# Kernel tuning notes

Hardware: AMD Instinct MI355X
Metric: run time of the kernel (lower is better)

## Reference

```python
import jax, jax.numpy as jnp
import numpy as np
import math

D, NH, DFF = 1024, 16, 4096
B, S = 2, 2048
EPS = 1e-5


def _mha(q_in, k_in, v_in, wq, bq, wk, bk, wv, bv, wo, bo, mask):
    Bq, Sq, Dm = q_in.shape
    Sk = k_in.shape[1]
    dh = Dm // NH
    q = (q_in @ wq + bq).reshape(Bq, Sq, NH, dh).transpose(0, 2, 1, 3)
    k = (k_in @ wk + bk).reshape(Bq, Sk, NH, dh).transpose(0, 2, 1, 3)
    v = (v_in @ wv + bv).reshape(Bq, Sk, NH, dh).transpose(0, 2, 1, 3)
    scores = jnp.einsum('bhqd,bhkd->bhqk', q, k) / math.sqrt(dh)
    scores = jnp.where(mask == 0, jnp.float32(-1e9), scores)
    w = jax.nn.softmax(scores, axis=-1)
    out = jnp.einsum('bhqk,bhkd->bhqd', w, v)
    out = out.transpose(0, 2, 1, 3).reshape(Bq, Sq, Dm)
    return out @ wo + bo


def _ln(x, g, b):
    mu = jnp.mean(x, axis=-1, keepdims=True)
    var = jnp.var(x, axis=-1, keepdims=True)
    return (x - mu) * jax.lax.rsqrt(var + EPS) * g + b


def setup_inputs() -> dict:
    key = jax.random.key(0)
    ks = jax.random.split(key, 20)
    sc = 1.0 / math.sqrt(D)
    inp = {
        'x': jax.random.normal(ks[0], (B, S, D), jnp.float32),
        'encoder_output': jax.random.normal(ks[1], (B, S, D), jnp.float32),
        'src_mask': jnp.ones((B, 1, 1, S), jnp.int32),
        'tgt_mask': jnp.tril(jnp.ones((S, S), jnp.int32))[None, None],
    }
    names = ['s_wq', 's_wk', 's_wv', 's_wo', 'c_wq', 'c_wk', 'c_wv', 'c_wo']
    for i, n in enumerate(names):
        inp[n] = jax.random.normal(ks[2 + i], (D, D), jnp.float32) * sc
        inp[n.replace('w', 'b')] = jnp.zeros((D,), jnp.float32)
    inp['ff_w1'] = jax.random.normal(ks[10], (D, DFF), jnp.float32) * sc
    inp['ff_b1'] = jnp.zeros((DFF,), jnp.float32)
    inp['ff_w2'] = jax.random.normal(ks[11], (DFF, D), jnp.float32) / math.sqrt(DFF)
    inp['ff_b2'] = jnp.zeros((D,), jnp.float32)
    for i in (1, 2, 3):
        inp[f'ln{i}_g'] = jnp.ones((D,), jnp.float32)
        inp[f'ln{i}_b'] = jnp.zeros((D,), jnp.float32)
    return inp


def reference(x, encoder_output, src_mask, tgt_mask,
              s_wq, s_bq, s_wk, s_bk, s_wv, s_bv, s_wo, s_bo,
              c_wq, c_bq, c_wk, c_bk, c_wv, c_bv, c_wo, c_bo,
              ff_w1, ff_b1, ff_w2, ff_b2,
              ln1_g, ln1_b, ln2_g, ln2_b, ln3_g, ln3_b):
    # self-attention + residual + LN (dropout is identity in eval)
    a = _mha(x, x, x, s_wq, s_bq, s_wk, s_bk, s_wv, s_bv, s_wo, s_bo, tgt_mask)
    x = _ln(x + a, ln1_g, ln1_b)
    # cross-attention
    a = _mha(x, encoder_output, encoder_output,
             c_wq, c_bq, c_wk, c_bk, c_wv, c_bv, c_wo, c_bo, src_mask)
    x = _ln(x + a, ln2_g, ln2_b)
    # FFN
    f = jax.nn.relu(x @ ff_w1 + ff_b1) @ ff_w2 + ff_b2
    return _ln(x + f, ln3_g, ln3_b)
```

## Files before the change

kernel.cpp:

```cpp
#include <hip/hip_runtime.h>
#include <hip/hip_bf16.h>
#include <stdint.h>


#define DEV static __device__ __forceinline__

typedef short bf16s;
typedef __attribute__((ext_vector_type(8))) short bf16x8;
typedef __attribute__((ext_vector_type(4))) float f32x4;

DEV short f2b(float f) {
    union { __hip_bfloat16 h; short s; } u;
    u.h = __float2bfloat16(f);
    return u.s;
}

DEV f32x4 mfma16(bf16x8 a, bf16x8 b, f32x4 c) {
    return __builtin_amdgcn_mfma_f32_16x16x32_bf16(a, b, c, 0, 0, 0);
}

DEV void gload_lds16(const bf16s* g, short* l) {
    __builtin_amdgcn_global_load_lds(
        (const __attribute__((address_space(1))) void*)g,
        (__attribute__((address_space(3))) void*)l,
        16, 0, 0);
}

__global__ __launch_bounds__(256) void cast2_f32_bf16_kernel(
    const float* __restrict__ a, const float* __restrict__ b,
    bf16s* __restrict__ out, int n)
{
    int i = (blockIdx.x * 256 + threadIdx.x) * 8;
    const float* src = (i < n) ? a : b;
    int j = (i < n) ? i : i - n;
    const float4 u = *(const float4*)(src + j);
    const float4 v = *(const float4*)(src + j + 4);
    bf16x8 r;
    r[0] = f2b(u.x); r[1] = f2b(u.y); r[2] = f2b(u.z); r[3] = f2b(u.w);
    r[4] = f2b(v.x); r[5] = f2b(v.y); r[6] = f2b(v.z); r[7] = f2b(v.w);
    *(bf16x8*)(out + i) = r;
}

struct P8 { const float* p[8]; };

__global__ __launch_bounds__(256) void transpose_cast8_kernel(
    P8 srcs, bf16s* __restrict__ dst)
{
    __shared__ short tile[64][65];
    const float* W = srcs.p[blockIdx.z];
    bf16s* Wt = dst + (size_t)blockIdx.z * 1024 * 1024;
    const int n0 = blockIdx.x * 64, k0 = blockIdx.y * 64;
    const int t = threadIdx.x;
#pragma unroll
    for (int it = 0; it < 16; ++it) {
        int idx = it * 256 + t;
        int r = idx >> 6, c = idx & 63;
        tile[r][c] = f2b(W[(size_t)(k0 + r) * 1024 + n0 + c]);
    }
    __syncthreads();
#pragma unroll
    for (int it = 0; it < 16; ++it) {
        int idx = it * 256 + t;
        int r = idx >> 6, c = idx & 63;
        Wt[(size_t)(n0 + r) * 1024 + k0 + c] = tile[c][r];
    }
}

__global__ __launch_bounds__(256) void transpose_cast_kernel(
    const float* __restrict__ W, bf16s* __restrict__ Wt, int Krows, int Ncols)
{
    __shared__ short tile[64][65];
    const int n0 = blockIdx.x * 64, k0 = blockIdx.y * 64;
    const int t = threadIdx.x;
#pragma unroll
    for (int it = 0; it < 16; ++it) {
        int idx = it * 256 + t;
        int r = idx >> 6, c = idx & 63;
        tile[r][c] = f2b(W[(size_t)(k0 + r) * Ncols + n0 + c]);
    }
    __syncthreads();
#pragma unroll
    for (int it = 0; it < 16; ++it) {
        int idx = it * 256 + t;
        int r = idx >> 6, c = idx & 63;
        Wt[(size_t)(n0 + r) * Krows + k0 + c] = tile[c][r];
    }
}

__global__ __launch_bounds__(256) void transpose_v_kernel(
    const bf16s* __restrict__ V, int ldv, bf16s* __restrict__ Vt, int Sk)
{
    __shared__ short tile[64][65];
    const int s0 = blockIdx.x * 64;
    const int bh = blockIdx.y, b = bh >> 4, h = bh & 15;
    const int t = threadIdx.x;
#pragma unroll
    for (int it = 0; it < 16; ++it) {
        int idx = it * 256 + t;
        int r = idx >> 6, c = idx & 63;
        tile[r][c] = V[(size_t)(b * Sk + s0 + r) * ldv + h * 64 + c];
    }
    __syncthreads();
#pragma unroll
    for (int it = 0; it < 16; ++it) {
        int idx = it * 256 + t;
        int r = idx >> 6, c = idx & 63;
        Vt[((size_t)bh * 64 + r) * Sk + s0 + c] = tile[c][r];
    }
}

__global__ void concat3_kernel(const float* a, const float* b, const float* c,
                               float* o, int n)
{
    int i = blockIdx.x * 256 + threadIdx.x;
    if (i < n) { o[i] = a[i]; o[n + i] = b[i]; o[2 * n + i] = c[i]; }
}
__global__ void concat2_kernel(const float* a, const float* b, float* o, int n)
{
    int i = blockIdx.x * 256 + threadIdx.x;
    if (i < n) { o[i] = a[i]; o[n + i] = b[i]; }
}

template<int BM, int OUT_BF16, int RELU>
__global__ __launch_bounds__(256, (BM == 64 ? 4 : 2))
void gemm_bt_kernel(const bf16s* __restrict__ A, const bf16s* __restrict__ Bt,
                    const float* __restrict__ bias, void* __restrict__ Cp,
                    int M, int N, int K)
{
    constexpr int BN = 128;
    constexpr int WR = BM / 64;
    constexpr int WC = 4 / WR;
    constexpr int TN = BN / WC;
    constexpr int NF = TN / 16;
    constexpr int RA = BM / 64;
    constexpr int ASZ = BM * 32;

    __shared__ short As[2 * ASZ];
    __shared__ short Bs[2 * BN * 32];

    const int t = threadIdx.x, lane = t & 63, wave = t >> 6;
    const int g = lane >> 4, ln16 = lane & 15;
    const int wr = wave / WC, wc = wave % WC;
    const int rowA0 = blockIdx.y * BM, rowB0 = blockIdx.x * BN;

    const bf16s* Ab = A + (size_t)rowA0 * K;
    const bf16s* Bb = Bt + (size_t)rowB0 * K;

    f32x4 acc[4][NF] = {};

    auto stage = [&](int buf, int k0) {
        short* Ad = As + buf * ASZ;
        short* Bd = Bs + buf * BN * 32;
#pragma unroll
        for (int rnd = 0; rnd < RA; ++rnd) {
            int p = rnd * 256 + t;
            int sr = p >> 3, c3 = (p & 7) ^ (sr & 7);
            int r = sr * 2 + (c3 >> 2), c = c3 & 3;
            gload_lds16(Ab + (size_t)r * K + k0 + c * 8,
                        Ad + (rnd * 256 + wave * 64) * 8);
        }
#pragma unroll
        for (int rnd = 0; rnd < 2; ++rnd) {
            int p = rnd * 256 + t;
            int sr = p >> 3, c3 = (p & 7) ^ (sr & 7);
            int r = sr * 2 + (c3 >> 2), c = c3 & 3;
            gload_lds16(Bb + (size_t)r * K + k0 + c * 8,
                        Bd + (rnd * 256 + wave * 64) * 8);
        }
    };

    stage(0, 0);
    __syncthreads();
    int cur = 0;
    for (int k0 = 0; k0 < K; k0 += 32) {
        if (k0 + 32 < K) stage(cur ^ 1, k0 + 32);
        const short* Ar = As + cur * ASZ;
        const short* Br = Bs + cur * BN * 32;
        bf16x8 af[4], bfr[NF];
#pragma unroll
        for (int m = 0; m < 4; ++m) {
            int r = wr * 64 + m * 16 + ln16;
            int sr = r >> 1, c3 = (r & 1) * 4 + g;
            af[m] = *(const bf16x8*)(Ar + sr * 64 + ((c3 ^ (sr & 7)) * 8));
        }
#pragma unroll
        for (int n = 0; n < NF; ++n) {
            int r = wc * TN + n * 16 + ln16;
            int sr = r >> 1, c3 = (r & 1) * 4 + g;
            bfr[n] = *(const bf16x8*)(Br + sr * 64 + ((c3 ^ (sr & 7)) * 8));
        }
#pragma unroll
        for (int m = 0; m < 4; ++m)
#pragma unroll
            for (int n = 0; n < NF; ++n)
                acc[m][n] = mfma16(af[m], bfr[n], acc[m][n]);
        __syncthreads();
        cur ^= 1;
    }

    const int row0 = rowA0 + wr * 64, col0 = rowB0 + wc * TN;
#pragma unroll
    for (int n = 0; n < NF; ++n) {
        const int col = col0 + n * 16 + ln16;
        const float bv = bias[col];
#pragma unroll
        for (int m = 0; m < 4; ++m) {
#pragma unroll
            for (int r = 0; r < 4; ++r) {
                int row = row0 + m * 16 + g * 4 + r;
                float v = acc[m][n][r] + bv;
                if (RELU) v = fmaxf(v, 0.f);
                if (OUT_BF16) ((bf16s*)Cp)[(size_t)row * N + col] = f2b(v);
                else          ((float*)Cp)[(size_t)row * N + col] = v;
            }
        }
    }
}

template<int CAUSAL>
__global__ __launch_bounds__(256, 4)
void flash_kernel(const bf16s* __restrict__ Q, int ldq,
                  const bf16s* __restrict__ K, int ldk,
                  const bf16s* __restrict__ Vt,
                  bf16s* __restrict__ O, int ldo,
                  int Sq, int Sk, float scale)
{
    __shared__ short Ks[2 * 64 * 64];
    __shared__ short Vs[2 * 64 * 64];
    __shared__ short Ps[4 * 16 * 64];
    const int t = threadIdx.x, lane = t & 63, wave = t >> 6;
    const int g = lane >> 4, ln16 = lane & 15;
    const int qt = CAUSAL ? (int)(gridDim.x - 1 - blockIdx.x) : (int)blockIdx.x;
    const int bh = blockIdx.y, b = bh >> 4, h = bh & 15;
    const int q0 = qt * 64;
    const float sc2 = scale * 1.44269504f;

    bf16x8 aq[2];
    {
        const size_t qrow = (size_t)(b * Sq + q0 + wave * 16 + ln16);
#pragma unroll
        for (int kk = 0; kk < 2; ++kk)
            aq[kk] = *(const bf16x8*)(Q + qrow * ldq + h * 64 + kk * 32 + g * 8);
    }

    float m_r[4], l_r[4];
    f32x4 oa[4] = {};
#pragma unroll
    for (int r = 0; r < 4; ++r) { m_r[r] = -1e30f; l_r[r] = 0.f; }

    const int nkt = CAUSAL ? (qt + 1) : (Sk >> 6);
    const bf16s* Kbase = K + (size_t)b * Sk * ldk + h * 64;
    const bf16s* Vbase = Vt + (size_t)bh * 64 * Sk;
    short* myP = Ps + wave * 1024;

    auto stage = [&](int buf, int kt) {
        const bf16s* ksrc = Kbase + (size_t)(kt * 64) * ldk;
        const bf16s* vsrc = Vbase + kt * 64;
        short* Kd = Ks + buf * 4096;
        short* Vd = Vs + buf * 4096;
#pragma unroll
        for (int rnd = 0; rnd < 2; ++rnd) {
            int p = rnd * 256 + t;
            int r = p >> 3, c = (p & 7) ^ (r & 7);
            gload_lds16(ksrc + (size_t)r * ldk + c * 8,
                        Kd + (rnd * 256 + wave * 64) * 8);
        }
#pragma unroll
        for (int rnd = 0; rnd < 2; ++rnd) {
            int p = rnd * 256 + t;
            int r = p >> 3, c = (p & 7) ^ (r & 7);
            gload_lds16(vsrc + (size_t)r * Sk + c * 8,
                        Vd + (rnd * 256 + wave * 64) * 8);
        }
    };

    stage(0, 0);
    __syncthreads();
    int cur = 0;

    for (int kt = 0; kt < nkt; ++kt) {
        if (kt + 1 < nkt) stage(cur ^ 1, kt + 1);
        const short* Kr = Ks + cur * 4096;
        const short* Vr = Vs + cur * 4096;

        f32x4 sa[4] = {};
#pragma unroll
        for (int kk = 0; kk < 2; ++kk) {
#pragma unroll
            for (int n = 0; n < 4; ++n) {
                int key = n * 16 + ln16;
                bf16x8 bk = *(const bf16x8*)(Kr + key * 64 +
                                             (((kk * 4 + g) ^ (key & 7)) * 8));
                sa[n] = mfma16(aq[kk], bk, sa[n]);
            }
        }

        const bool diag = CAUSAL && (kt == qt);
        float sv[4][4];
#pragma unroll
        for (int n = 0; n < 4; ++n) {
#pragma unroll
            for (int r = 0; r < 4; ++r) {
                float s = sa[n][r] * sc2;
                if (diag) {
                    int kl = n * 16 + ln16, ql = wave * 16 + g * 4 + r;
                    if (kl > ql) s = -1e30f;
                }
                sv[n][r] = s;
            }
        }

        float rm[4];
#pragma unroll
        for (int r = 0; r < 4; ++r)
            rm[r] = fmaxf(fmaxf(sv[0][r], sv[1][r]), fmaxf(sv[2][r], sv[3][r]));
#pragma unroll
        for (int x = 1; x < 16; x <<= 1)
#pragma unroll
            for (int r = 0; r < 4; ++r)
                rm[r] = fmaxf(rm[r], __shfl_xor(rm[r], x, 64));

        float al[4];
#pragma unroll
        for (int r = 0; r < 4; ++r) {
            float mn = fmaxf(m_r[r], rm[r]);
            al[r] = exp2f(m_r[r] - mn);
            m_r[r] = mn;
        }
        float rs[4] = {0.f, 0.f, 0.f, 0.f};
#pragma unroll
        for (int n = 0; n < 4; ++n)
#pragma unroll
            for (int r = 0; r < 4; ++r) {
                float p = exp2f(sv[n][r] - m_r[r]);
                sv[n][r] = p;
                rs[r] += p;
            }
#pragma unroll
        for (int x = 1; x < 16; x <<= 1)
#pragma unroll
            for (int r = 0; r < 4; ++r)
                rs[r] += __shfl_xor(rs[r], x, 64);
#pragma unroll
        for (int r = 0; r < 4; ++r)
            l_r[r] = l_r[r] * al[r] + rs[r];

#pragma unroll
        for (int n = 0; n < 4; ++n)
#pragma unroll
            for (int r = 0; r < 4; ++r) {
                int row = g * 4 + r, col = n * 16 + ln16;
                myP[row * 64 + (((col >> 3) ^ (row & 7)) * 8) + (col & 7)] =
                    f2b(sv[n][r]);
            }
        asm volatile("s_waitcnt lgkmcnt(0)" ::: "memory");

#pragma unroll
        for (int n = 0; n < 4; ++n)
#pragma unroll
            for (int r = 0; r < 4; ++r)
                oa[n][r] *= al[r];
#pragma unroll
        for (int kk = 0; kk < 2; ++kk) {
            bf16x8 pa = *(const bf16x8*)(myP + ln16 * 64 +
                                         (((kk * 4 + g) ^ (ln16 & 7)) * 8));
#pragma unroll
            for (int n = 0; n < 4; ++n) {
                int d = n * 16 + ln16;
                bf16x8 vb = *(const bf16x8*)(Vr + d * 64 +
                                             (((kk * 4 + g) ^ (d & 7)) * 8));
                oa[n] = mfma16(pa, vb, oa[n]);
            }
        }
        __syncthreads();
        cur ^= 1;
    }

    float inv[4];
#pragma unroll
    for (int r = 0; r < 4; ++r) inv[r] = 1.f / l_r[r];
#pragma unroll
    for (int n = 0; n < 4; ++n)
#pragma unroll
        for (int r = 0; r < 4; ++r) {
            int q = q0 + wave * 16 + g * 4 + r;
            int d = h * 64 + n * 16 + ln16;
            O[(size_t)(b * Sq + q) * ldo + d] = f2b(oa[n][r] * inv[r]);
        }
}

template<int WRITE_BF16>
__global__ __launch_bounds__(256)
void add_ln_kernel(const float* __restrict__ X, const float* __restrict__ A,
                   const float* __restrict__ G, const float* __restrict__ Bb,
                   float* __restrict__ Y, bf16s* __restrict__ Yb)
{
    const int row = blockIdx.x, t = threadIdx.x;
    const int lane = t & 63, w = t >> 6;
    const size_t base = (size_t)row * 1024 + t * 4;
    const float4 xv = *(const float4*)(X + base);
    const float4 av = *(const float4*)(A + base);
    float4 v;
    v.x = xv.x + av.x; v.y = xv.y + av.y; v.z = xv.z + av.z; v.w = xv.w + av.w;
    float s = v.x + v.y + v.z + v.w;
    float q = v.x * v.x + v.y * v.y + v.z * v.z + v.w * v.w;
#pragma unroll
    for (int x = 1; x < 64; x <<= 1) {
        s += __shfl_xor(s, x, 64);
        q += __shfl_xor(q, x, 64);
    }
    __shared__ float red[8];
    if (lane == 0) { red[w] = s; red[4 + w] = q; }
    __syncthreads();
    s = red[0] + red[1] + red[2] + red[3];
    q = red[4] + red[5] + red[6] + red[7];
    const float mu = s * (1.f / 1024.f);
    const float var = q * (1.f / 1024.f) - mu * mu;
    const float rstd = rsqrtf(var + 1e-5f);
    const float4 gv = *(const float4*)(G + t * 4);
    const float4 bv = *(const float4*)(Bb + t * 4);
    float o0 = (v.x - mu) * rstd * gv.x + bv.x;
    float o1 = (v.y - mu) * rstd * gv.y + bv.y;
    float o2 = (v.z - mu) * rstd * gv.z + bv.z;
    float o3 = (v.w - mu) * rstd * gv.w + bv.w;
    float4 ov; ov.x = o0; ov.y = o1; ov.z = o2; ov.w = o3;
    *(float4*)(Y + base) = ov;
    if (WRITE_BF16) {
        short4 yb;
        yb.x = f2b(o0); yb.y = f2b(o1); yb.z = f2b(o2); yb.w = f2b(o3);
        *(short4*)(Yb + base) = yb;
    }
}

extern "C" void kernel_launch(void* const* d_in, const int* in_sizes, int n_in,
                              void* d_out, int out_size, void* d_ws, size_t ws_size,
                              hipStream_t stream)
{
    constexpr int Dm = 1024, DFF = 4096, Bq = 2, S = 2048;
    constexpr int NT = Bq * S;
    constexpr size_t MM = (size_t)Dm * Dm;

    const float* x    = (const float*)d_in[0];
    const float* enc  = (const float*)d_in[1];
    const float* s_wq = (const float*)d_in[4];  const float* s_bq = (const float*)d_in[5];
    const float* s_wk = (const float*)d_in[6];  const float* s_bk = (const float*)d_in[7];
    const float* s_wv = (const float*)d_in[8];  const float* s_bv = (const float*)d_in[9];
    const float* s_wo = (const float*)d_in[10]; const float* s_bo = (const float*)d_in[11];
    const float* c_wq = (const float*)d_in[12]; const float* c_bq = (const float*)d_in[13];
    const float* c_wk = (const float*)d_in[14]; const float* c_bk = (const float*)d_in[15];
    const float* c_wv = (const float*)d_in[16]; const float* c_bv = (const float*)d_in[17];
    const float* c_wo = (const float*)d_in[18]; const float* c_bo = (const float*)d_in[19];
    const float* ffw1 = (const float*)d_in[20]; const float* ffb1 = (const float*)d_in[21];
    const float* ffw2 = (const float*)d_in[22]; const float* ffb2 = (const float*)d_in[23];
    const float* ln1g = (const float*)d_in[24]; const float* ln1b = (const float*)d_in[25];
    const float* ln2g = (const float*)d_in[26]; const float* ln2b = (const float*)d_in[27];
    const float* ln3g = (const float*)d_in[28]; const float* ln3b = (const float*)d_in[29];

    char* ws = (char*)d_ws;
    size_t off = 0;
    auto alloc = [&](size_t bytes) -> char* {
        char* p = ws + off;
        off += (bytes + 255) & ~(size_t)255;
        return p;
    };

    bf16s* xbf   = (bf16s*)alloc((size_t)NT * Dm * 2);
    bf16s* encbf = (bf16s*)alloc((size_t)NT * Dm * 2);
    bf16s* wAll  = (bf16s*)alloc(8 * MM * 2);
    bf16s* w1T   = (bf16s*)alloc((size_t)Dm * DFF * 2);
    bf16s* w2T   = (bf16s*)alloc((size_t)Dm * DFF * 2);
    float* bqkv  = (float*)alloc((size_t)3 * Dm * 4);
    float* bkvc  = (float*)alloc((size_t)2 * Dm * 4);
    bf16s* QKV   = (bf16s*)alloc((size_t)NT * 3 * Dm * 2);
    bf16s* Vt    = (bf16s*)alloc((size_t)NT * Dm * 2);
    bf16s* AO    = (bf16s*)alloc((size_t)NT * Dm * 2);
    float* Pbuf  = (float*)alloc((size_t)NT * Dm * 4);
    float* x1f   = (float*)alloc((size_t)NT * Dm * 4);
    bf16s* x1bf  = (bf16s*)alloc((size_t)NT * Dm * 2);
    float* x2f   = (float*)alloc((size_t)NT * Dm * 4);
    bf16s* x2bf  = (bf16s*)alloc((size_t)NT * Dm * 2);
    bf16s* Hbuf  = (bf16s*)alloc((size_t)NT * DFF * 2);
    (void)ws_size; (void)in_sizes; (void)n_in; (void)out_size;

    bf16s* wqkvT = wAll;
    bf16s* woTs  = wAll + 3 * MM;
    bf16s* wqTc  = wAll + 4 * MM;
    bf16s* wkvTc = wAll + 5 * MM;
    bf16s* woTc  = wAll + 7 * MM;

    cast2_f32_bf16_kernel<<<2 * NT * Dm / 8 / 256, 256, 0, stream>>>(
        x, enc, xbf, NT * Dm);
    P8 srcs = {{s_wq, s_wk, s_wv, s_wo, c_wq, c_wk, c_wv, c_wo}};
    transpose_cast8_kernel<<<dim3(16, 16, 8), 256, 0, stream>>>(srcs, wAll);
    transpose_cast_kernel<<<dim3(64, 16), 256, 0, stream>>>(ffw1, w1T, Dm, DFF);
    transpose_cast_kernel<<<dim3(16, 64), 256, 0, stream>>>(ffw2, w2T, DFF, Dm);
    concat3_kernel<<<4, 256, 0, stream>>>(s_bq, s_bk, s_bv, bqkv, Dm);
    concat2_kernel<<<4, 256, 0, stream>>>(c_bk, c_bv, bkvc, Dm);

    gemm_bt_kernel<128, 1, 0><<<dim3(24, 32), 256, 0, stream>>>(
        xbf, wqkvT, bqkv, QKV, NT, 3 * Dm, Dm);
    transpose_v_kernel<<<dim3(32, 32), 256, 0, stream>>>(
        QKV + 2 * Dm, 3 * Dm, Vt, S);
    flash_kernel<1><<<dim3(32, 32), 256, 0, stream>>>(
        QKV, 3 * Dm, QKV + Dm, 3 * Dm, Vt, AO, Dm, S, S, 0.125f);
    gemm_bt_kernel<64, 0, 0><<<dim3(8, 64), 256, 0, stream>>>(
        AO, woTs, s_bo, Pbuf, NT, Dm, Dm);
    add_ln_kernel<1><<<NT, 256, 0, stream>>>(x, Pbuf, ln1g, ln1b, x1f, x1bf);

    bf16s* Q2  = QKV;
    bf16s* KV2 = QKV + (size_t)NT * Dm;
    gemm_bt_kernel<64, 1, 0><<<dim3(8, 64), 256, 0, stream>>>(
        x1bf, wqTc, c_bq, Q2, NT, Dm, Dm);
    gemm_bt_kernel<128, 1, 0><<<dim3(16, 32), 256, 0, stream>>>(
        encbf, wkvTc, bkvc, KV2, NT, 2 * Dm, Dm);
    transpose_v_kernel<<<dim3(32, 32), 256, 0, stream>>>(
        KV2 + Dm, 2 * Dm, Vt, S);
    flash_kernel<0><<<dim3(32, 32), 256, 0, stream>>>(
        Q2, Dm, KV2, 2 * Dm, Vt, AO, Dm, S, S, 0.125f);
    gemm_bt_kernel<64, 0, 0><<<dim3(8, 64), 256, 0, stream>>>(
        AO, woTc, c_bo, Pbuf, NT, Dm, Dm);
    add_ln_kernel<1><<<NT, 256, 0, stream>>>(x1f, Pbuf, ln2g, ln2b, x2f, x2bf);

    gemm_bt_kernel<128, 1, 1><<<dim3(32, 32), 256, 0, stream>>>(
        x2bf, w1T, ffb1, Hbuf, NT, DFF, Dm);
    gemm_bt_kernel<64, 0, 0><<<dim3(8, 64), 256, 0, stream>>>(
        Hbuf, w2T, ffb2, Pbuf, NT, Dm, DFF);
    add_ln_kernel<0><<<NT, 256, 0, stream>>>(
        x2f, Pbuf, ln3g, ln3b, (float*)d_out, nullptr);
}
```

Measured before the change: 694.7 us.

## Compute transposed S in attention so softmax reductions become per-lane

The QK^T MFMA now swaps its operands, so each lane holds a key column for one query row. Row max and row sum then need only two cross-lane shuffles instead of four per register, and the scale is folded into an fma inside exp2. P is written to LDS as packed bf16 pairs (8-byte stores) instead of scalar shorts, and s_setprio is raised around the MFMA blocks. The rescale and normalisation factors must be broadcast back to the output layout with __shfl, which adds some cross-lane traffic.

```diff
diff --git a/kernel.cpp b/kernel.cpp
--- a/kernel.cpp
+++ b/kernel.cpp
@@ -13,6 +13,12 @@
     union { __hip_bfloat16 h; short s; } u;
     u.h = __float2bfloat16(f);
     return u.s;
+}
+
+DEV unsigned pk2(float lo, float hi) {
+    union { __hip_bfloat162 h; unsigned u; } u;
+    u.h = __float22bfloat162_rn(float2{lo, hi});
+    return u.u;
 }
 
 DEV f32x4 mfma16(bf16x8 a, bf16x8 b, f32x4 c) {
@@ -243,10 +249,8 @@
             aq[kk] = *(const bf16x8*)(Q + qrow * ldq + h * 64 + kk * 32 + g * 8);
     }
 
-    float m_r[4], l_r[4];
+    float m_raw = -1e30f, l_sum = 0.f;
     f32x4 oa[4] = {};
-#pragma unroll
-    for (int r = 0; r < 4; ++r) { m_r[r] = -1e30f; l_r[r] = 0.f; }
 
     const int nkt = CAUSAL ? (qt + 1) : (Sk >> 6);
     const bf16s* Kbase = K + (size_t)b * Sk * ldk + h * 64;
@@ -284,82 +288,78 @@
         const short* Vr = Vs + cur * 4096;
 
         f32x4 sa[4] = {};
+        __builtin_amdgcn_s_setprio(1);
 #pragma unroll
         for (int kk = 0; kk < 2; ++kk) {
 #pragma unroll
             for (int n = 0; n < 4; ++n) {
                 int key = n * 16 + ln16;
-                bf16x8 bk = *(const bf16x8*)(Kr + key * 64 +
+                bf16x8 ak = *(const bf16x8*)(Kr + key * 64 +
                                              (((kk * 4 + g) ^ (key & 7)) * 8));
-                sa[n] = mfma16(aq[kk], bk, sa[n]);
+                sa[n] = mfma16(ak, aq[kk], sa[n]);
             }
         }
-
+        __builtin_amdgcn_s_setprio(0);
+
+        float sv[4][4];
         const bool diag = CAUSAL && (kt == qt);
-        float sv[4][4];
-#pragma unroll
-        for (int n = 0; n < 4; ++n) {
+#pragma unroll
+        for (int n = 0; n < 4; ++n)
 #pragma unroll
             for (int r = 0; r < 4; ++r) {
-                float s = sa[n][r] * sc2;
-                if (diag) {
-                    int kl = n * 16 + ln16, ql = wave * 16 + g * 4 + r;
-                    if (kl > ql) s = -1e30f;
-                }
+                float s = sa[n][r];
+                if (diag && (n * 16 + g * 4 + r > wave * 16 + ln16)) s = -1e30f;
                 sv[n][r] = s;
             }
-        }
-
-        float rm[4];
+
+        float rm = fmaxf(
+            fmaxf(fmaxf(fmaxf(sv[0][0], sv[0][1]), fmaxf(sv[0][2], sv[0][3])),
+                  fmaxf(fmaxf(sv[1][0], sv[1][1]), fmaxf(sv[1][2], sv[1][3]))),
+            fmaxf(fmaxf(fmaxf(sv[2][0], sv[2][1]), fmaxf(sv[2][2], sv[2][3])),
+                  fmaxf(fmaxf(sv[3][0], sv[3][1]), fmaxf(sv[3][2], sv[3][3]))));
+        rm = fmaxf(rm, __shfl_xor(rm, 16, 64));
+        rm = fmaxf(rm, __shfl_xor(rm, 32, 64));
+
+        const float mnew = fmaxf(m_raw, rm);
+        const float al = exp2f((m_raw - mnew) * sc2);
+        m_raw = mnew;
+        const float nm = -mnew * sc2;
+
+        float rs = 0.f;
+#pragma unroll
+        for (int n = 0; n < 4; ++n)
+#pragma unroll
+            for (int r = 0; r < 4; ++r) {
+                float p = exp2f(fmaf(sv[n][r], sc2, nm));
+                sv[n][r] = p;
+                rs += p;
+            }
+        rs += __shfl_xor(rs, 16, 64);
+        rs += __shfl_xor(rs, 32, 64);
+        l_sum = l_sum * al + rs;
+
+        float alr[4];
 #pragma unroll
         for (int r = 0; r < 4; ++r)
-            rm[r] = fmaxf(fmaxf(sv[0][r], sv[1][r]), fmaxf(sv[2][r], sv[3][r]));
-#pragma unroll
-        for (int x = 1; x < 16; x <<= 1)
+            alr[r] = __shfl(al, g * 4 + r, 64);
+#pragma unroll
+        for (int n = 0; n < 4; ++n)
 #pragma unroll
             for (int r = 0; r < 4; ++r)
-                rm[r] = fmaxf(rm[r], __shfl_xor(rm[r], x, 64));
-
-        float al[4];
-#pragma unroll
-        for (int r = 0; r < 4; ++r) {
-            float mn = fmaxf(m_r[r], rm[r]);
-            al[r] = exp2f(m_r[r] - mn);
-            m_r[r] = mn;
-        }
-        float rs[4] = {0.f, 0.f, 0.f, 0.f};
-#pragma unroll
-        for (int n = 0; n < 4; ++n)
-#pragma unroll
-            for (int r = 0; r < 4; ++r) {
-                float p = exp2f(sv[n][r] - m_r[r]);
-                sv[n][r] = p;
-                rs[r] += p;
-            }
-#pragma unroll
-        for (int x = 1; x < 16; x <<= 1)
-#pragma unroll
-            for (int r = 0; r < 4; ++r)
-                rs[r] += __shfl_xor(rs[r], x, 64);
-#pragma unroll
-        for (int r = 0; r < 4; ++r)
-            l_r[r] = l_r[r] * al[r] + rs[r];
-
-#pragma unroll
-        for (int n = 0; n < 4; ++n)
-#pragma unroll
-            for (int r = 0; r < 4; ++r) {
-                int row = g * 4 + r, col = n * 16 + ln16;
-                myP[row * 64 + (((col >> 3) ^ (row & 7)) * 8) + (col & 7)] =
-                    f2b(sv[n][r]);
-            }
+                oa[n][r] *= alr[r];
+
+#pragma unroll
+        for (int n = 0; n < 4; ++n) {
+            uint2 w;
+            w.x = pk2(sv[n][0], sv[n][1]);
+            w.y = pk2(sv[n][2], sv[n][3]);
+            int c = n * 2 + (g >> 1);
+            int sh = ln16 * 64 + ((c ^ (ln16 & 7)) * 8) + (g & 1) * 4;
+            *(uint2*)(myP + sh) = w;
+        }
         asm volatile("s_waitcnt lgkmcnt(0)" ::: "memory");
 
-#pragma unroll
-        for (int n = 0; n < 4; ++n)
-#pragma unroll
-            for (int r = 0; r < 4; ++r)
-                oa[n][r] *= al[r];
+        __builtin_amdgcn_s_setprio(1);
 #pragma unroll
         for (int kk = 0; kk < 2; ++kk) {
             bf16x8 pa = *(const bf16x8*)(myP + ln16 * 64 +
@@ -372,20 +372,23 @@
                 oa[n] = mfma16(pa, vb, oa[n]);
             }
         }
+        __builtin_amdgcn_s_setprio(0);
         __syncthreads();
         cur ^= 1;
     }
 
-    float inv[4];
-#pragma unroll
-    for (int r = 0; r < 4; ++r) inv[r] = 1.f / l_r[r];
+    const float inv = 1.f / l_sum;
+    float invr[4];
+#pragma unroll
+    for (int r = 0; r < 4; ++r)
+        invr[r] = __shfl(inv, g * 4 + r, 64);
 #pragma unroll
     for (int n = 0; n < 4; ++n)
 #pragma unroll
         for (int r = 0; r < 4; ++r) {
             int q = q0 + wave * 16 + g * 4 + r;
             int d = h * 64 + n * 16 + ln16;
-            O[(size_t)(b * Sq + q) * ldo + d] = f2b(oa[n][r] * inv[r]);
+            O[(size_t)(b * Sq + q) * ldo + d] = f2b(oa[n][r] * invr[r]);
         }
 }
 
```

New measurement: 625.6 us. 1.11x faster.
